# Kernel optimization log

Measured on AMD Instinct MI355X. Metric: run time of the kernel, lower is better.

The kernel has to match this reference:

```python
import jax, jax.numpy as jnp
import numpy as np

N = 100000   # nodes
D = 128      # feature dim
E = 1600000  # edges (avg degree 16)
BN_EPS = 1e-5


def setup_inputs() -> dict:
    key = jax.random.key(0)
    ks = jax.random.split(key, 8)
    x = jax.random.normal(ks[0], (N, D), dtype=jnp.float32)
    edge_index = jax.random.randint(ks[1], (2, E), 0, N, dtype=jnp.int64)
    W = jax.random.normal(ks[2], (D, D), dtype=jnp.float32) * 0.05   # GCNConv linear weight
    b = jax.random.normal(ks[3], (D,), dtype=jnp.float32) * 0.05     # GCNConv bias
    gamma = jax.random.uniform(ks[4], (D,), dtype=jnp.float32) + 0.5 # BN weight
    beta = jax.random.normal(ks[5], (D,), dtype=jnp.float32) * 0.1   # BN bias
    running_mean = jax.random.normal(ks[6], (D,), dtype=jnp.float32) * 0.1
    running_var = jax.random.uniform(ks[7], (D,), dtype=jnp.float32) + 0.5
    return {"x": x, "edge_index": edge_index, "W": W, "b": b,
            "gamma": gamma, "beta": beta,
            "running_mean": running_mean, "running_var": running_var}


def reference(x, edge_index, W, b, gamma, beta, running_mean, running_var):
    # --- GCNConv (default: add self-loops, symmetric normalization) ---
    h = x @ W                                        # [N, D]
    loops = jnp.arange(N, dtype=edge_index.dtype)
    src = jnp.concatenate([edge_index[0], loops])    # [E+N]
    dst = jnp.concatenate([edge_index[1], loops])    # [E+N]
    deg = jax.ops.segment_sum(jnp.ones_like(dst, dtype=h.dtype), dst, num_segments=N)
    dinv = jax.lax.rsqrt(jnp.maximum(deg, 1.0))      # deg >= 1 due to self-loops
    norm = dinv[src] * dinv[dst]                     # [E+N]
    agg = jax.ops.segment_sum(h[src] * norm[:, None], dst, num_segments=N)  # [N, D]
    agg = agg + b
    # --- BatchNorm1d (inference: running stats) ---
    bn = (agg - running_mean) * jax.lax.rsqrt(running_var + BN_EPS) * gamma + beta
    # --- ReLU + residual (dropout is identity in eval) ---
    return jax.nn.relu(bn) + x
```

## Files before the change

### kernel.cpp

```cpp
#include <hip/hip_runtime.h>

#define D 128
#define BN_EPS 1e-5f
#define NBUCK 512
#define BSHIFT 8
#define BNODES 256
#define CAP 4608

using short8 = __attribute__((ext_vector_type(8))) short;
using floatx4 = __attribute__((ext_vector_type(4))) float;

__device__ inline unsigned short f2bf(float f) {
    unsigned u = __float_as_uint(f);
    u += 0x7fff + ((u >> 16) & 1);
    return (unsigned short)(u >> 16);
}
__device__ inline float bf2f(unsigned short s) {
    return __uint_as_float(((unsigned)s) << 16);
}

__global__ __launch_bounds__(256) void init_kernel(
    const float* __restrict__ W, const float* __restrict__ b,
    const float* __restrict__ gamma, const float* __restrict__ beta,
    const float* __restrict__ mean, const float* __restrict__ var,
    unsigned short* __restrict__ Wt, float* __restrict__ scv,
    float* __restrict__ pov, int* __restrict__ resCnt) {
    int t = blockIdx.x * 256 + threadIdx.x;
    Wt[(size_t)(t & 127) * D + (t >> 7)] = f2bf(W[t]);
    if (t < NBUCK) resCnt[t] = 0;
    if (t < D) {
        float sc = gamma[t] * rsqrtf(var[t] + BN_EPS);
        scv[t] = sc;
        pov[t] = (b[t] - mean[t]) * sc + beta[t];
    }
}

__global__ __launch_bounds__(512) void pB_kernel(const int* __restrict__ src,
                                                 const int* __restrict__ dst,
                                                 int* __restrict__ resCnt,
                                                 unsigned int* __restrict__ pairs,
                                                 int E) {
    __shared__ int lh[NBUCK];
    __shared__ int lcur[NBUCK];
    int tid = threadIdx.x;
    lh[tid] = 0;
    __syncthreads();
    int chunk = (E + gridDim.x - 1) / gridDim.x;
    int base = blockIdx.x * chunk;
    int lim = min(chunk, E - base);
    if (lim <= 0) return;
    for (int i = tid; i < lim; i += 512) atomicAdd(&lh[dst[base + i] >> BSHIFT], 1);
    __syncthreads();
    int c = lh[tid];
    lcur[tid] = tid * CAP + (c ? atomicAdd(&resCnt[tid], c) : 0);
    __syncthreads();
    for (int i = tid; i < lim; i += 512) {
        int s = src[base + i], d2 = dst[base + i];
        int b2 = d2 >> BSHIFT;
        int pos = atomicAdd(&lcur[b2], 1);
        if (pos < (b2 + 1) * CAP)
            pairs[pos] = (((unsigned)d2 & 255u) << 24) | (unsigned)s;
    }
}

__global__ __launch_bounds__(512) void sortxs_kernel(
    const unsigned int* __restrict__ pairs, const int* __restrict__ resCnt,
    const int* __restrict__ src, const int* __restrict__ dst,
    const float* __restrict__ x, int* __restrict__ deg, int* __restrict__ offs,
    int* __restrict__ colidx, float* __restrict__ dinv,
    unsigned short* __restrict__ xs, int N, int E) {
    __shared__ int sb[NBUCK];
    __shared__ int lh[BNODES];
    __shared__ int lcur[BNODES];
    __shared__ float sdv[BNODES];
    int tid = threadIdx.x;
    int b = blockIdx.x;
    sb[tid] = resCnt[tid];
    __syncthreads();
    for (int d = 1; d < NBUCK; d <<= 1) {
        int v = (tid >= d) ? sb[tid - d] : 0;
        __syncthreads();
        sb[tid] += v;
        __syncthreads();
    }
    int cnt = resCnt[b];
    int cbase = sb[b] - cnt;
    int pbase = b * CAP;
    if (tid < BNODES) lh[tid] = 0;
    __syncthreads();

    if (cnt <= CAP) {
        for (int i = tid; i < cnt; i += 512)
            atomicAdd(&lh[pairs[pbase + i] >> 24], 1);
        __syncthreads();
        int orig = (tid < BNODES) ? lh[tid] : 0;
        for (int d = 1; d < BNODES; d <<= 1) {
            int v = (tid < BNODES && tid >= d) ? lh[tid - d] : 0;
            __syncthreads();
            if (tid < BNODES) lh[tid] += v;
            __syncthreads();
        }
        if (tid < BNODES) {
            int exc = lh[tid] - orig;
            int node = b * BNODES + tid;
            float dvv = rsqrtf((float)(orig + 1));
            sdv[tid] = dvv;
            if (node < N) {
                deg[node] = orig;
                offs[node] = cbase + exc;
                dinv[node] = dvv;
            }
            lcur[tid] = exc;
        }
        __syncthreads();
        for (int i = tid; i < cnt; i += 512) {
            unsigned int p = pairs[pbase + i];
            int pos = atomicAdd(&lcur[p >> 24], 1);
            colidx[cbase + pos] = (int)(p & 0x00FFFFFFu);
        }
    } else {
        for (int i = tid; i < E; i += 512) {
            int d2 = dst[i];
            if ((d2 >> BSHIFT) == b) atomicAdd(&lh[d2 & 255], 1);
        }
        __syncthreads();
        if (tid < BNODES) {
            int orig = lh[tid];
            int node = b * BNODES + tid;
            float dvv = rsqrtf((float)(orig + 1));
            sdv[tid] = dvv;
            if (node < N) {
                deg[node] = orig;
                offs[node] = -1;
                dinv[node] = dvv;
            }
        }
        __syncthreads();
    }

    int nb = min(BNODES, N - b * BNODES);
    if (nb > 0) {
        const float4* x4 = (const float4*)x;
        ushort4* xs4 = (ushort4*)xs;
        int tot = nb * 32;
        for (int c2 = tid; c2 < tot; c2 += 512) {
            int nl = c2 >> 5, q = c2 & 31;
            int node = b * BNODES + nl;
            float dvv = sdv[nl];
            float4 f = x4[(size_t)node * 32 + q];
            ushort4 o;
            o.x = f2bf(dvv * f.x); o.y = f2bf(dvv * f.y);
            o.z = f2bf(dvv * f.z); o.w = f2bf(dvv * f.w);
            xs4[(size_t)node * 32 + q] = o;
        }
    }
}

__global__ void wt_kernel(const float* __restrict__ W, const float* __restrict__ b,
                          const float* __restrict__ gamma, const float* __restrict__ beta,
                          const float* __restrict__ mean, const float* __restrict__ var,
                          unsigned short* __restrict__ Wt, float* __restrict__ scv,
                          float* __restrict__ pov) {
    int t = blockIdx.x * blockDim.x + threadIdx.x;
    int k = t >> 7, n = t & 127;
    Wt[(size_t)n * D + k] = f2bf(W[t]);
    if (t < D) {
        float sc = gamma[t] * rsqrtf(var[t] + BN_EPS);
        scv[t] = sc;
        pov[t] = (b[t] - mean[t]) * sc + beta[t];
    }
}

__global__ void deg_kernel(const int* __restrict__ dst, int* __restrict__ deg, int E) {
    int e = blockIdx.x * blockDim.x + threadIdx.x;
    if (e < E) atomicAdd(&deg[dst[e]], 1);
}

__global__ void dinv_kernel(const int* __restrict__ deg, float* __restrict__ dinv, int N) {
    int v = blockIdx.x * blockDim.x + threadIdx.x;
    if (v < N) dinv[v] = rsqrtf((float)(deg[v] + 1));
}

__global__ __launch_bounds__(256) void scan1_kernel(const int* __restrict__ deg,
                                                    int* __restrict__ bsum, int N) {
    __shared__ int s[256];
    int t = threadIdx.x;
    int v = blockIdx.x * 256 + t;
    s[t] = (v < N) ? deg[v] : 0;
    for (int st = 128; st > 0; st >>= 1) {
        __syncthreads();
        if (t < st) s[t] += s[t + st];
    }
    if (t == 0) bsum[blockIdx.x] = s[0];
}

__global__ __launch_bounds__(512) void scan2_kernel(int* __restrict__ bsum,
                                                    int* __restrict__ offs, int P, int N) {
    __shared__ int a[512];
    int t = threadIdx.x;
    int orig = (t < P) ? bsum[t] : 0;
    a[t] = orig;
    __syncthreads();
    for (int d = 1; d < 512; d <<= 1) {
        int tv = (t >= d) ? a[t - d] : 0;
        __syncthreads();
        a[t] += tv;
        __syncthreads();
    }
    if (t < P) bsum[t] = a[t] - orig;
    if (t == 0) offs[N] = a[511];
}

__global__ __launch_bounds__(256) void scan3_kernel(const int* __restrict__ deg,
                                                    const int* __restrict__ bsum,
                                                    int* __restrict__ offs,
                                                    int* __restrict__ cursor, int N) {
    __shared__ int a[256];
    int t = threadIdx.x;
    int v = blockIdx.x * 256 + t;
    int d = (v < N) ? deg[v] : 0;
    a[t] = d;
    __syncthreads();
    for (int st = 1; st < 256; st <<= 1) {
        int tv = (t >= st) ? a[t - st] : 0;
        __syncthreads();
        a[t] += tv;
        __syncthreads();
    }
    if (v < N) {
        int off = bsum[blockIdx.x] + a[t] - d;
        offs[v] = off;
        cursor[v] = off;
    }
}

__global__ void fill_kernel(const int* __restrict__ src, const int* __restrict__ dst,
                            int* __restrict__ cursor, int* __restrict__ colidx, int E) {
    int e = blockIdx.x * blockDim.x + threadIdx.x;
    if (e < E) {
        int d = dst[e];
        int pos = atomicAdd(&cursor[d], 1);
        colidx[pos] = src[e];
    }
}

__global__ __launch_bounds__(256) void agg_kernel(
    const float* __restrict__ x, const unsigned short* __restrict__ xs,
    const float* __restrict__ dinv, const int* __restrict__ offs,
    const int* __restrict__ deg, const int* __restrict__ colidx,
    const int* __restrict__ src, const int* __restrict__ dst,
    float* __restrict__ outp, unsigned int* __restrict__ aggb, int N, int E) {
    int wid = (blockIdx.x * blockDim.x + threadIdx.x) >> 6;
    if (wid >= N) return;
    int lane = threadIdx.x & 63;
    float dv = dinv[wid];
    float a0, a1;
    int p = offs[wid];
    if (xs) {
        const unsigned int* xs32 = (const unsigned int*)xs;
        unsigned int sv = xs32[(size_t)wid * 64 + lane];
        a0 = bf2f((unsigned short)sv);
        a1 = bf2f((unsigned short)(sv >> 16));
        if (p >= 0) {
            int pe = p + deg[wid];
            for (; p + 16 <= pe; p += 16) {
                int u[16];
                unsigned int v[16];
#pragma unroll
                for (int j = 0; j < 16; ++j) u[j] = colidx[p + j];
#pragma unroll
                for (int j = 0; j < 16; ++j) v[j] = xs32[(size_t)u[j] * 64 + lane];
#pragma unroll
                for (int j = 0; j < 16; ++j) {
                    a0 += bf2f((unsigned short)v[j]);
                    a1 += bf2f((unsigned short)(v[j] >> 16));
                }
            }
            for (; p + 4 <= pe; p += 4) {
                int u[4];
                unsigned int v[4];
#pragma unroll
                for (int j = 0; j < 4; ++j) u[j] = colidx[p + j];
#pragma unroll
                for (int j = 0; j < 4; ++j) v[j] = xs32[(size_t)u[j] * 64 + lane];
#pragma unroll
                for (int j = 0; j < 4; ++j) {
                    a0 += bf2f((unsigned short)v[j]);
                    a1 += bf2f((unsigned short)(v[j] >> 16));
                }
            }
            for (; p < pe; ++p) {
                unsigned int v = xs32[(size_t)colidx[p] * 64 + lane];
                a0 += bf2f((unsigned short)v);
                a1 += bf2f((unsigned short)(v >> 16));
            }
        } else {
            for (int e = 0; e < E; ++e) {
                if (dst[e] == wid) {
                    unsigned int v = xs32[(size_t)src[e] * 64 + lane];
                    a0 += bf2f((unsigned short)v);
                    a1 += bf2f((unsigned short)(v >> 16));
                }
            }
        }
        aggb[(size_t)wid * 64 + lane] =
            (unsigned int)f2bf(dv * a0) | ((unsigned int)f2bf(dv * a1) << 16);
    } else {
        const float2* x2 = (const float2*)x;
        float2 s = x2[(size_t)wid * 64 + lane];
        a0 = dv * s.x;
        a1 = dv * s.y;
        int pe = p + deg[wid];
        for (; p < pe; ++p) {
            int u = colidx[p];
            float du = dinv[u];
            float2 vv = x2[(size_t)u * 64 + lane];
            a0 += du * vv.x;
            a1 += du * vv.y;
        }
        float2 r;
        r.x = dv * a0;
        r.y = dv * a1;
        ((float2*)outp)[(size_t)wid * 64 + lane] = r;
    }
}

__global__ __launch_bounds__(256) void gemm_kernel(
    float* __restrict__ outp, const float* __restrict__ xg,
    const unsigned short* __restrict__ Wt, const unsigned short* __restrict__ aggb,
    const float* __restrict__ scv, const float* __restrict__ pov, int nTiles) {
    __shared__ uint4 sW4[2048];
    int tid = threadIdx.x;
    const uint4* W4 = (const uint4*)Wt;
#pragma unroll
    for (int i = 0; i < 8; ++i) {
        int q = tid + i * 256;
        int row = q >> 4, c4 = q & 15;
        sW4[row * 16 + (c4 ^ (row & 7))] = W4[q];
    }
    __syncthreads();

    int wid = (blockIdx.x * blockDim.x + tid) >> 6;
    if (wid >= nTiles) return;
    int lane = tid & 63;
    int m = lane & 15, quad = lane >> 4;
    int row0 = wid * 16;

    short8 A[4];
    if (aggb) {
        const unsigned short* arow = aggb + (size_t)(row0 + m) * D;
#pragma unroll
        for (int ks = 0; ks < 4; ++ks)
            A[ks] = *(const short8*)&arow[ks * 32 + quad * 8];
    } else {
        const float* arow = outp + (size_t)(row0 + m) * D;
#pragma unroll
        for (int ks = 0; ks < 4; ++ks) {
            float4 f0 = *(const float4*)(arow + ks * 32 + quad * 8);
            float4 f1 = *(const float4*)(arow + ks * 32 + quad * 8 + 4);
            short8 af;
            af[0] = (short)f2bf(f0.x); af[1] = (short)f2bf(f0.y);
            af[2] = (short)f2bf(f0.z); af[3] = (short)f2bf(f0.w);
            af[4] = (short)f2bf(f1.x); af[5] = (short)f2bf(f1.y);
            af[6] = (short)f2bf(f1.z); af[7] = (short)f2bf(f1.w);
            A[ks] = af;
        }
    }

#pragma unroll
    for (int cg2 = 0; cg2 < 8; ++cg2) {
        int brow = cg2 * 16 + m;
        floatx4 acc = {0.f, 0.f, 0.f, 0.f};
#pragma unroll
        for (int ks = 0; ks < 4; ++ks) {
            short8 Bf = *(const short8*)&sW4[brow * 16 + ((ks * 4 + quad) ^ (m & 7))];
            acc = __builtin_amdgcn_mfma_f32_16x16x32_bf16(A[ks], Bf, acc, 0, 0, 0);
        }
        int col = cg2 * 16 + m;
        float sc = scv[col], po = pov[col];
#pragma unroll
        for (int i = 0; i < 4; ++i) {
            int row = row0 + quad * 4 + i;
            float bn = acc[i] * sc + po;
            size_t idx = (size_t)row * D + col;
            outp[idx] = fmaxf(bn, 0.f) + xg[idx];
        }
    }
}

extern "C" void kernel_launch(void* const* d_in, const int* in_sizes, int n_in,
                              void* d_out, int out_size, void* d_ws, size_t ws_size,
                              hipStream_t stream) {
    const float* x = (const float*)d_in[0];
    const int* edge = (const int*)d_in[1];
    const float* Wm = (const float*)d_in[2];
    const float* b = (const float*)d_in[3];
    const float* gamma = (const float*)d_in[4];
    const float* beta = (const float*)d_in[5];
    const float* mean = (const float*)d_in[6];
    const float* var = (const float*)d_in[7];
    float* out = (float*)d_out;

    int N = in_sizes[0] / D;
    int E = in_sizes[1] / 2;
    const int* src = edge;
    const int* dst = edge + E;
    int P = (N + 255) / 256;

    char* w = (char*)d_ws;
    size_t cur = 0;
    auto take = [&](size_t bytes) -> void* {
        cur = (cur + 15) & ~(size_t)15;
        void* p = w + cur;
        cur += bytes;
        return p;
    };
    int* deg = (int*)take((size_t)N * 4);
    int* resCnt = (int*)take(NBUCK * 4);
    float* dinv = (float*)take((size_t)N * 4);
    int* offs = (int*)take((size_t)(N + 1) * 4);
    int* cursor = (int*)take((size_t)N * 4);
    int* bsum = (int*)take((size_t)(P + 1) * 4);
    unsigned short* Wt = (unsigned short*)take((size_t)D * D * 2);
    float* scv = (float*)take(D * 4);
    float* pov = (float*)take(D * 4);
    int* colidx = (int*)take((size_t)E * 4);
    cur = (cur + 15) & ~(size_t)15;
    size_t fixedEnd = cur;

    size_t xsBytes = (size_t)N * D * 2;
    size_t pairsBytes = (size_t)NBUCK * CAP * 4;
    size_t zoneBytes = (xsBytes > pairsBytes) ? xsBytes : pairsBytes;
    bool fast = (fixedEnd + xsBytes + zoneBytes <= ws_size) && (N < (1 << 24));

    unsigned short* xs = nullptr;
    unsigned int* pairs = nullptr;
    unsigned int* aggb = nullptr;
    if (fast) {
        xs = (unsigned short*)(w + fixedEnd);
        pairs = (unsigned int*)(w + fixedEnd + xsBytes);
        aggb = (unsigned int*)(w + fixedEnd + xsBytes);
    }

    if (fast) {
        init_kernel<<<(D * D) / 256, 256, 0, stream>>>(Wm, b, gamma, beta, mean, var,
                                                       Wt, scv, pov, resCnt);
        pB_kernel<<<128, 512, 0, stream>>>(src, dst, resCnt, pairs, E);
        sortxs_kernel<<<NBUCK, 512, 0, stream>>>(pairs, resCnt, src, dst, x, deg, offs,
                                                 colidx, dinv, xs, N, E);
        agg_kernel<<<(N * 64 + 255) / 256, 256, 0, stream>>>(
            x, xs, dinv, offs, deg, colidx, src, dst, out, aggb, N, E);
        int nTiles = (N + 15) / 16;
        gemm_kernel<<<(nTiles * 64 + 255) / 256, 256, 0, stream>>>(
            out, x, Wt, (const unsigned short*)aggb, scv, pov, nTiles);
    } else {
        wt_kernel<<<(D * D) / 256, 256, 0, stream>>>(Wm, b, gamma, beta, mean, var, Wt,
                                                     scv, pov);
        hipMemsetAsync(deg, 0, sizeof(int) * N, stream);
        deg_kernel<<<(E + 255) / 256, 256, 0, stream>>>(dst, deg, E);
        dinv_kernel<<<(N + 255) / 256, 256, 0, stream>>>(deg, dinv, N);
        scan1_kernel<<<P, 256, 0, stream>>>(deg, bsum, N);
        scan2_kernel<<<1, 512, 0, stream>>>(bsum, offs, P, N);
        scan3_kernel<<<P, 256, 0, stream>>>(deg, bsum, offs, cursor, N);
        fill_kernel<<<(E + 255) / 256, 256, 0, stream>>>(src, dst, cursor, colidx, E);
        agg_kernel<<<(N * 64 + 255) / 256, 256, 0, stream>>>(
            x, nullptr, dinv, offs, deg, colidx, src, dst, out, nullptr, N, E);
        int nTiles = (N + 15) / 16;
        gemm_kernel<<<(nTiles * 64 + 255) / 256, 256, 0, stream>>>(out, x, Wt, nullptr,
                                                                   scv, pov, nTiles);
    }
}
```

Baseline: 263.8 us.

## Fuse neighbor aggregation and bf16 MFMA GEMM into one kernel

Replaces the separate aggregation and GEMM launches on the fast path with one kernel. Each 1024-thread block aggregates 16 nodes (one wave per node) into a shared-memory bf16 tile, then 8 waves each compute a 16-column slice with MFMA and write the BN/ReLU/residual output. This removes the round trip of the aggregated bf16 matrix through global memory and one launch. In exchange, each wave reloads its W slice from global memory with no LDS staging, and the block barrier makes every wave wait for the slowest node's gather, which can lower gather throughput.

After: 281.4 us. +6.7%, slower.

```diff
diff --git a/kernel.cpp b/kernel.cpp
--- a/kernel.cpp
+++ b/kernel.cpp
@@ -156,6 +156,104 @@
     }
 }
 
+__global__ __launch_bounds__(1024, 8) void aggemm_kernel(
+    const unsigned short* __restrict__ xs, const float* __restrict__ dinv,
+    const int* __restrict__ offs, const int* __restrict__ deg,
+    const int* __restrict__ colidx, const int* __restrict__ src,
+    const int* __restrict__ dst, const float* __restrict__ xg,
+    const unsigned short* __restrict__ Wt, const float* __restrict__ scv,
+    const float* __restrict__ pov, float* __restrict__ outp, int N, int E) {
+    __shared__ unsigned int sA[16][68];
+    int tid = threadIdx.x;
+    int lane = tid & 63;
+    int w = tid >> 6;
+    int row0 = blockIdx.x * 16;
+    int node = row0 + w;
+    const unsigned int* xs32 = (const unsigned int*)xs;
+
+    if (node < N) {
+        float dv = dinv[node];
+        unsigned int sv = xs32[(size_t)node * 64 + lane];
+        float a0 = bf2f((unsigned short)sv);
+        float a1 = bf2f((unsigned short)(sv >> 16));
+        int p = offs[node];
+        if (p >= 0) {
+            int pe = p + deg[node];
+            for (; p + 16 <= pe; p += 16) {
+                int u[16];
+                unsigned int v[16];
+#pragma unroll
+                for (int j = 0; j < 16; ++j) u[j] = colidx[p + j];
+#pragma unroll
+                for (int j = 0; j < 16; ++j) v[j] = xs32[(size_t)u[j] * 64 + lane];
+#pragma unroll
+                for (int j = 0; j < 16; ++j) {
+                    a0 += bf2f((unsigned short)v[j]);
+                    a1 += bf2f((unsigned short)(v[j] >> 16));
+                }
+            }
+            for (; p + 4 <= pe; p += 4) {
+                int u[4];
+                unsigned int v[4];
+#pragma unroll
+                for (int j = 0; j < 4; ++j) u[j] = colidx[p + j];
+#pragma unroll
+                for (int j = 0; j < 4; ++j) v[j] = xs32[(size_t)u[j] * 64 + lane];
+#pragma unroll
+                for (int j = 0; j < 4; ++j) {
+                    a0 += bf2f((unsigned short)v[j]);
+                    a1 += bf2f((unsigned short)(v[j] >> 16));
+                }
+            }
+            for (; p < pe; ++p) {
+                unsigned int v = xs32[(size_t)colidx[p] * 64 + lane];
+                a0 += bf2f((unsigned short)v);
+                a1 += bf2f((unsigned short)(v >> 16));
+            }
+        } else {
+            for (int e = 0; e < E; ++e) {
+                if (dst[e] == node) {
+                    unsigned int v = xs32[(size_t)src[e] * 64 + lane];
+                    a0 += bf2f((unsigned short)v);
+                    a1 += bf2f((unsigned short)(v >> 16));
+                }
+            }
+        }
+        sA[w][lane] =
+            (unsigned int)f2bf(dv * a0) | ((unsigned int)f2bf(dv * a1) << 16);
+    } else {
+        sA[w][lane] = 0u;
+    }
+    __syncthreads();
+
+    if (w < 8) {
+        int m = lane & 15, quad = lane >> 4;
+        short8 B[4];
+#pragma unroll
+        for (int ks = 0; ks < 4; ++ks)
+            B[ks] = *(const short8*)&Wt[(size_t)(w * 16 + m) * D + ks * 32 + quad * 8];
+        short8 A[4];
+#pragma unroll
+        for (int ks = 0; ks < 4; ++ks)
+            A[ks] = *(const short8*)&sA[m][ks * 16 + quad * 4];
+        floatx4 acc = {0.f, 0.f, 0.f, 0.f};
+#pragma unroll
+        for (int ks = 0; ks < 4; ++ks)
+            acc = __builtin_amdgcn_mfma_f32_16x16x32_bf16(A[ks], B[ks], acc, 0, 0, 0);
+        int col = w * 16 + m;
+        float sc = scv[col], po = pov[col];
+#pragma unroll
+        for (int i = 0; i < 4; ++i) {
+            int row = row0 + quad * 4 + i;
+            if (row < N) {
+                float bn = acc[i] * sc + po;
+                size_t idx = (size_t)row * D + col;
+                outp[idx] = fmaxf(bn, 0.f) + xg[idx];
+            }
+        }
+    }
+}
+
 __global__ void wt_kernel(const float* __restrict__ W, const float* __restrict__ b,
                           const float* __restrict__ gamma, const float* __restrict__ beta,
                           const float* __restrict__ mean, const float* __restrict__ var,
@@ -245,90 +343,36 @@
 }
 
 __global__ __launch_bounds__(256) void agg_kernel(
-    const float* __restrict__ x, const unsigned short* __restrict__ xs,
-    const float* __restrict__ dinv, const int* __restrict__ offs,
-    const int* __restrict__ deg, const int* __restrict__ colidx,
-    const int* __restrict__ src, const int* __restrict__ dst,
-    float* __restrict__ outp, unsigned int* __restrict__ aggb, int N, int E) {
+    const float* __restrict__ x, const float* __restrict__ dinv,
+    const int* __restrict__ offs, const int* __restrict__ deg,
+    const int* __restrict__ colidx, float* __restrict__ outp, int N) {
     int wid = (blockIdx.x * blockDim.x + threadIdx.x) >> 6;
     if (wid >= N) return;
     int lane = threadIdx.x & 63;
     float dv = dinv[wid];
-    float a0, a1;
     int p = offs[wid];
-    if (xs) {
-        const unsigned int* xs32 = (const unsigned int*)xs;
-        unsigned int sv = xs32[(size_t)wid * 64 + lane];
-        a0 = bf2f((unsigned short)sv);
-        a1 = bf2f((unsigned short)(sv >> 16));
-        if (p >= 0) {
-            int pe = p + deg[wid];
-            for (; p + 16 <= pe; p += 16) {
-                int u[16];
-                unsigned int v[16];
-#pragma unroll
-                for (int j = 0; j < 16; ++j) u[j] = colidx[p + j];
-#pragma unroll
-                for (int j = 0; j < 16; ++j) v[j] = xs32[(size_t)u[j] * 64 + lane];
-#pragma unroll
-                for (int j = 0; j < 16; ++j) {
-                    a0 += bf2f((unsigned short)v[j]);
-                    a1 += bf2f((unsigned short)(v[j] >> 16));
-                }
-            }
-            for (; p + 4 <= pe; p += 4) {
-                int u[4];
-                unsigned int v[4];
-#pragma unroll
-                for (int j = 0; j < 4; ++j) u[j] = colidx[p + j];
-#pragma unroll
-                for (int j = 0; j < 4; ++j) v[j] = xs32[(size_t)u[j] * 64 + lane];
-#pragma unroll
-                for (int j = 0; j < 4; ++j) {
-                    a0 += bf2f((unsigned short)v[j]);
-                    a1 += bf2f((unsigned short)(v[j] >> 16));
-                }
-            }
-            for (; p < pe; ++p) {
-                unsigned int v = xs32[(size_t)colidx[p] * 64 + lane];
-                a0 += bf2f((unsigned short)v);
-                a1 += bf2f((unsigned short)(v >> 16));
-            }
-        } else {
-            for (int e = 0; e < E; ++e) {
-                if (dst[e] == wid) {
-                    unsigned int v = xs32[(size_t)src[e] * 64 + lane];
-                    a0 += bf2f((unsigned short)v);
-                    a1 += bf2f((unsigned short)(v >> 16));
-                }
-            }
-        }
-        aggb[(size_t)wid * 64 + lane] =
-            (unsigned int)f2bf(dv * a0) | ((unsigned int)f2bf(dv * a1) << 16);
-    } else {
-        const float2* x2 = (const float2*)x;
-        float2 s = x2[(size_t)wid * 64 + lane];
-        a0 = dv * s.x;
-        a1 = dv * s.y;
-        int pe = p + deg[wid];
-        for (; p < pe; ++p) {
-            int u = colidx[p];
-            float du = dinv[u];
-            float2 vv = x2[(size_t)u * 64 + lane];
-            a0 += du * vv.x;
-            a1 += du * vv.y;
-        }
-        float2 r;
-        r.x = dv * a0;
-        r.y = dv * a1;
-        ((float2*)outp)[(size_t)wid * 64 + lane] = r;
-    }
+    int pe = p + deg[wid];
+    const float2* x2 = (const float2*)x;
+    float2 s = x2[(size_t)wid * 64 + lane];
+    float a0 = dv * s.x;
+    float a1 = dv * s.y;
+    for (; p < pe; ++p) {
+        int u = colidx[p];
+        float du = dinv[u];
+        float2 vv = x2[(size_t)u * 64 + lane];
+        a0 += du * vv.x;
+        a1 += du * vv.y;
+    }
+    float2 r;
+    r.x = dv * a0;
+    r.y = dv * a1;
+    ((float2*)outp)[(size_t)wid * 64 + lane] = r;
 }
 
 __global__ __launch_bounds__(256) void gemm_kernel(
     float* __restrict__ outp, const float* __restrict__ xg,
-    const unsigned short* __restrict__ Wt, const unsigned short* __restrict__ aggb,
-    const float* __restrict__ scv, const float* __restrict__ pov, int nTiles) {
+    const unsigned short* __restrict__ Wt, const float* __restrict__ scv,
+    const float* __restrict__ pov, int nTiles) {
     __shared__ uint4 sW4[2048];
     int tid = threadIdx.x;
     const uint4* W4 = (const uint4*)Wt;
@@ -347,24 +391,17 @@
     int row0 = wid * 16;
 
     short8 A[4];
-    if (aggb) {
-        const unsigned short* arow = aggb + (size_t)(row0 + m) * D;
-#pragma unroll
-        for (int ks = 0; ks < 4; ++ks)
-            A[ks] = *(const short8*)&arow[ks * 32 + quad * 8];
-    } else {
-        const float* arow = outp + (size_t)(row0 + m) * D;
-#pragma unroll
-        for (int ks = 0; ks < 4; ++ks) {
-            float4 f0 = *(const float4*)(arow + ks * 32 + quad * 8);
-            float4 f1 = *(const float4*)(arow + ks * 32 + quad * 8 + 4);
-            short8 af;
-            af[0] = (short)f2bf(f0.x); af[1] = (short)f2bf(f0.y);
-            af[2] = (short)f2bf(f0.z); af[3] = (short)f2bf(f0.w);
-            af[4] = (short)f2bf(f1.x); af[5] = (short)f2bf(f1.y);
-            af[6] = (short)f2bf(f1.z); af[7] = (short)f2bf(f1.w);
-            A[ks] = af;
-        }
+    const float* arow = outp + (size_t)(row0 + m) * D;
+#pragma unroll
+    for (int ks = 0; ks < 4; ++ks) {
+        float4 f0 = *(const float4*)(arow + ks * 32 + quad * 8);
+        float4 f1 = *(const float4*)(arow + ks * 32 + quad * 8 + 4);
+        short8 af;
+        af[0] = (short)f2bf(f0.x); af[1] = (short)f2bf(f0.y);
+        af[2] = (short)f2bf(f0.z); af[3] = (short)f2bf(f0.w);
+        af[4] = (short)f2bf(f1.x); af[5] = (short)f2bf(f1.y);
+        af[6] = (short)f2bf(f1.z); af[7] = (short)f2bf(f1.w);
+        A[ks] = af;
     }
 
 #pragma unroll
@@ -435,11 +472,9 @@
 
     unsigned short* xs = nullptr;
     unsigned int* pairs = nullptr;
-    unsigned int* aggb = nullptr;
     if (fast) {
         xs = (unsigned short*)(w + fixedEnd);
         pairs = (unsigned int*)(w + fixedEnd + xsBytes);
-        aggb = (unsigned int*)(w + fixedEnd + xsBytes);
     }
 
     if (fast) {
@@ -448,11 +483,8 @@
         pB_kernel<<<128, 512, 0, stream>>>(src, dst, resCnt, pairs, E);
         sortxs_kernel<<<NBUCK, 512, 0, stream>>>(pairs, resCnt, src, dst, x, deg, offs,
                                                  colidx, dinv, xs, N, E);
-        agg_kernel<<<(N * 64 + 255) / 256, 256, 0, stream>>>(
-            x, xs, dinv, offs, deg, colidx, src, dst, out, aggb, N, E);
-        int nTiles = (N + 15) / 16;
-        gemm_kernel<<<(nTiles * 64 + 255) / 256, 256, 0, stream>>>(
-            out, x, Wt, (const unsigned short*)aggb, scv, pov, nTiles);
+        aggemm_kernel<<<(N + 15) / 16, 1024, 0, stream>>>(
+            xs, dinv, offs, deg, colidx, src, dst, x, Wt, scv, pov, out, N, E);
     } else {
         wt_kernel<<<(D * D) / 256, 256, 0, stream>>>(Wm, b, gamma, beta, mean, var, Wt,
                                                      scv, pov);
@@ -463,10 +495,10 @@
         scan2_kernel<<<1, 512, 0, stream>>>(bsum, offs, P, N);
         scan3_kernel<<<P, 256, 0, stream>>>(deg, bsum, offs, cursor, N);
         fill_kernel<<<(E + 255) / 256, 256, 0, stream>>>(src, dst, cursor, colidx, E);
-        agg_kernel<<<(N * 64 + 255) / 256, 256, 0, stream>>>(
-            x, nullptr, dinv, offs, deg, colidx, src, dst, out, nullptr, N, E);
+        agg_kernel<<<(N * 64 + 255) / 256, 256, 0, stream>>>(x, dinv, offs, deg, colidx,
+                                                             out, N);
         int nTiles = (N + 15) / 16;
-        gemm_kernel<<<(nTiles * 64 + 255) / 256, 256, 0, stream>>>(out, x, Wt, nullptr,
-                                                                   scv, pov, nTiles);
-    }
-}
+        gemm_kernel<<<(nTiles * 64 + 255) / 256, 256, 0, stream>>>(out, x, Wt, scv, pov,
+                                                                   nTiles);
+    }
+}
```

## Stage bucket partition in LDS for coalesced pair writes in pB_kernel

Applied to the files above, without the earlier changes.

The bucket-partition kernel now does a local prefix scan over bucket counts, scatters each edge's packed pair into shared memory in bucket order, and then writes the chunk to global memory in contiguous runs per bucket. This is meant to replace scattered global stores with mostly coalesced ones. The grid also grows from 128 blocks to enough blocks that each chunk fits in the shared staging buffer (PBCHUNK entries). In exchange it uses about 37KB of LDS per block, adds a scan and extra barriers, and issues more global atomics on resCnt because there are more blocks.

Result: faster. 253.4 us (-4.0%).

```diff
diff --git a/kernel.cpp b/kernel.cpp
--- a/kernel.cpp
+++ b/kernel.cpp
@@ -6,6 +6,7 @@
 #define BSHIFT 8
 #define BNODES 256
 #define CAP 4608
+#define PBCHUNK 6272
 
 using short8 = __attribute__((ext_vector_type(8))) short;
 using floatx4 = __attribute__((ext_vector_type(4))) float;
@@ -41,7 +42,10 @@
                                                  unsigned int* __restrict__ pairs,
                                                  int E) {
     __shared__ int lh[NBUCK];
-    __shared__ int lcur[NBUCK];
+    __shared__ int excl[NBUCK];
+    __shared__ int resBase[NBUCK];
+    __shared__ unsigned int ord[PBCHUNK];
+    __shared__ unsigned short bkt[PBCHUNK];
     int tid = threadIdx.x;
     lh[tid] = 0;
     __syncthreads();
@@ -52,14 +56,32 @@
     for (int i = tid; i < lim; i += 512) atomicAdd(&lh[dst[base + i] >> BSHIFT], 1);
     __syncthreads();
     int c = lh[tid];
-    lcur[tid] = tid * CAP + (c ? atomicAdd(&resCnt[tid], c) : 0);
+    excl[tid] = c;
+    __syncthreads();
+    for (int d = 1; d < NBUCK; d <<= 1) {
+        int v = (tid >= d) ? excl[tid - d] : 0;
+        __syncthreads();
+        excl[tid] += v;
+        __syncthreads();
+    }
+    int myExcl = excl[tid] - c;
+    resBase[tid] = tid * CAP + (c ? atomicAdd(&resCnt[tid], c) : 0);
+    __syncthreads();
+    excl[tid] = myExcl;
+    lh[tid] = myExcl;
     __syncthreads();
     for (int i = tid; i < lim; i += 512) {
         int s = src[base + i], d2 = dst[base + i];
         int b2 = d2 >> BSHIFT;
-        int pos = atomicAdd(&lcur[b2], 1);
-        if (pos < (b2 + 1) * CAP)
-            pairs[pos] = (((unsigned)d2 & 255u) << 24) | (unsigned)s;
+        int pos = atomicAdd(&lh[b2], 1);
+        ord[pos] = (((unsigned)d2 & 255u) << 24) | (unsigned)s;
+        bkt[pos] = (unsigned short)b2;
+    }
+    __syncthreads();
+    for (int i = tid; i < lim; i += 512) {
+        int b2 = bkt[i];
+        int dest = resBase[b2] + (i - excl[b2]);
+        if (dest < (b2 + 1) * CAP) pairs[dest] = ord[i];
     }
 }
 
@@ -443,9 +465,10 @@
     }
 
     if (fast) {
+        int pgrid = (E + PBCHUNK - 1) / PBCHUNK;
         init_kernel<<<(D * D) / 256, 256, 0, stream>>>(Wm, b, gamma, beta, mean, var,
                                                        Wt, scv, pov, resCnt);
-        pB_kernel<<<128, 512, 0, stream>>>(src, dst, resCnt, pairs, E);
+        pB_kernel<<<pgrid, 512, 0, stream>>>(src, dst, resCnt, pairs, E);
         sortxs_kernel<<<NBUCK, 512, 0, stream>>>(pairs, resCnt, src, dst, x, deg, offs,
                                                  colidx, dinv, xs, N, E);
         agg_kernel<<<(N * 64 + 255) / 256, 256, 0, stream>>>(
```
